# Kernel tuning notes

Hardware: AMD Instinct MI355X
Metric: run time of the kernel (lower is better)

Reference implementation:

```python
import jax, jax.numpy as jnp
import numpy as np

B, S, FEAT, HID, H = 8, 1024, 1024, 1024, 8
DH = HID // H  # head dim = 128
MASK_VAL = -128.0  # mask_val = -2**7 (soft additive mask, per original code)


def setup_inputs() -> dict:
    key = jax.random.key(0)
    ks = jax.random.split(key, 4)
    scale = 0.02
    return {
        "queries": jax.random.normal(ks[0], (B, S, FEAT), dtype=jnp.float32),
        "Wq": jax.random.normal(ks[1], (FEAT, HID), dtype=jnp.float32) * scale,
        "bq": jnp.zeros((HID,), dtype=jnp.float32),
        "Wk": jax.random.normal(ks[2], (FEAT, HID), dtype=jnp.float32) * scale,
        "bk": jnp.zeros((HID,), dtype=jnp.float32),
        "Wv": jax.random.normal(ks[3], (FEAT, HID), dtype=jnp.float32) * scale,
        "bv": jnp.zeros((HID,), dtype=jnp.float32),
    }


def reference(queries, Wq, bq, Wk, bk, Wv, bv):
    # Self-attention: keys = values = queries (torch forward defaults)
    q = queries @ Wq + bq  # [B,S,HID]
    k = queries @ Wk + bk
    v = queries @ Wv + bv
    # split heads: chunk along last dim == reshape (B,S,H,DH)
    qh = q.reshape(B, S, H, DH)
    kh = k.reshape(B, S, H, DH)
    vh = v.reshape(B, S, H, DH)
    # exp-scaled-dot score (non-standard: exp BEFORE mask/softmax)
    logits = jnp.einsum("bqhd,bkhd->bhqk", qh, kh) / np.float32(np.sqrt(DH))
    score = jnp.exp(logits)
    # soft additive causal mask: upper triangle (diag=1) gets -128
    mask = jnp.triu(jnp.full((S, S), MASK_VAL, dtype=score.dtype), k=1)
    att = jax.nn.softmax(score + mask, axis=-1)  # [B,H,S,S]
    ctx = jnp.einsum("bhqk,bkhd->bqhd", att, vh)  # [B,S,H,DH]
    # reverse heads: concat along last dim
    return ctx.reshape(B, S, HID)
```

## Files before the change

kernel.cpp:

```cpp
#include <hip/hip_runtime.h>


typedef __bf16 bf16x8 __attribute__((ext_vector_type(8)));
typedef float floatx4 __attribute__((ext_vector_type(4)));
typedef unsigned short u16;

#define RSCALE 0.08838834764831845f

__device__ __forceinline__ u16 f2b(float f) {
  union { float f; unsigned u; } v; v.f = f;
  return (u16)((v.u + 0x7FFFu + ((v.u >> 16) & 1u)) >> 16);
}

__device__ __forceinline__ void gld_lds16(const void* g, void* l) {
  __builtin_amdgcn_global_load_lds(
      (const __attribute__((address_space(1))) unsigned*)g,
      (__attribute__((address_space(3))) unsigned*)l, 16, 0, 0);
}

#define MFMA16(a, b, c) __builtin_amdgcn_mfma_f32_16x16x32_bf16(a, b, c, 0, 0, 0)

__global__ __launch_bounds__(256) void cast_x_kernel(const float4* __restrict__ X,
                                                     u16* __restrict__ Xb) {
  unsigned i = blockIdx.x * 256u + threadIdx.x;
  float4 v = X[i];
  ushort4 o;
  o.x = f2b(v.x); o.y = f2b(v.y); o.z = f2b(v.z); o.w = f2b(v.w);
  *reinterpret_cast<ushort4*>(Xb + 4u * i) = o;
}

__global__ __launch_bounds__(256) void transpose_w_kernel(
    const float* __restrict__ Wq, const float* __restrict__ Wk,
    const float* __restrict__ Wv, u16* __restrict__ Wtb) {
  const float* W = (blockIdx.z == 0) ? Wq : (blockIdx.z == 1) ? Wk : Wv;
  u16* Wt = Wtb + (size_t)blockIdx.z * (1024u * 1024u);
  __shared__ u16 tile[32][33];
  const int x = threadIdx.x, y = threadIdx.y;
  const int kt = blockIdx.x * 32, nt = blockIdx.y * 32;
#pragma unroll
  for (int i = 0; i < 4; ++i)
    tile[y + 8 * i][x] = f2b(W[(size_t)(kt + y + 8 * i) * 1024 + nt + x]);
  __syncthreads();
#pragma unroll
  for (int i = 0; i < 4; ++i)
    Wt[(size_t)(nt + y + 8 * i) * 1024 + kt + x] = tile[x][y + 8 * i];
}

__global__ __launch_bounds__(256) void gemm_qkv_kernel(
    const u16* __restrict__ Xb, const u16* __restrict__ Wtb,
    const float* __restrict__ bq, const float* __restrict__ bk,
    const float* __restrict__ bv, u16* __restrict__ Qh, u16* __restrict__ Kh,
    u16* __restrict__ Vt) {
  const int mat = blockIdx.z;
  const u16* __restrict__ Wt = Wtb + (size_t)mat * (1024u * 1024u);
  const float* __restrict__ bias = (mat == 0) ? bq : (mat == 1) ? bk : bv;

  const int m0 = blockIdx.x * 128;
  const int n0 = blockIdx.y * 128;

  __shared__ u16 As[128 * 32];
  __shared__ u16 Bs[128 * 32];

  const int tid = threadIdx.x;
  const int wid = tid >> 6;
  const int lane = tid & 63;
  const int quad = lane >> 4;
  const int l16 = lane & 15;
  const int wm = (wid & 1) * 64;
  const int wn = (wid >> 1) * 64;

  const floatx4 z4 = {0.f, 0.f, 0.f, 0.f};
  floatx4 acc[4][4];
#pragma unroll
  for (int i = 0; i < 4; ++i)
#pragma unroll
    for (int j = 0; j < 4; ++j) acc[i][j] = z4;

  const int rbase = wid * 32;
  for (int k0 = 0; k0 < 1024; k0 += 32) {
    __syncthreads();
#pragma unroll
    for (int c = 0; c < 2; ++c) {
      const int row = rbase + c * 16 + (lane >> 2);
      const int kk = k0 + (lane & 3) * 8;
      gld_lds16(Xb + (size_t)(m0 + row) * 1024 + kk, As + (rbase + c * 16) * 32);
      gld_lds16(Wt + (size_t)(n0 + row) * 1024 + kk, Bs + (rbase + c * 16) * 32);
    }
    __syncthreads();

    bf16x8 af[4], bfr[4];
#pragma unroll
    for (int i = 0; i < 4; ++i)
      af[i] = *(const bf16x8*)(As + (wm + i * 16 + l16) * 32 + quad * 8);
#pragma unroll
    for (int j = 0; j < 4; ++j)
      bfr[j] = *(const bf16x8*)(Bs + (wn + j * 16 + l16) * 32 + quad * 8);
#pragma unroll
    for (int i = 0; i < 4; ++i)
#pragma unroll
      for (int j = 0; j < 4; ++j) acc[i][j] = MFMA16(af[i], bfr[j], acc[i][j]);
  }

  const int b = m0 >> 10;
  const int h = n0 >> 7;
  const int sbase = (m0 & 1023) + wm;
  float bv4[4];
#pragma unroll
  for (int j = 0; j < 4; ++j) bv4[j] = bias[n0 + wn + j * 16 + l16];

  if (mat < 2) {
    u16* outp = (mat == 0 ? Qh : Kh) + (size_t)(b * 8 + h) * 1024 * 128;
#pragma unroll
    for (int i = 0; i < 4; ++i)
#pragma unroll
      for (int j = 0; j < 4; ++j) {
        const int d = wn + j * 16 + l16;
#pragma unroll
        for (int r = 0; r < 4; ++r) {
          const int s = sbase + i * 16 + quad * 4 + r;
          outp[(size_t)s * 128 + d] = f2b(acc[i][j][r] + bv4[j]);
        }
      }
  } else {
    u16* outp = Vt + (size_t)(b * 8 + h) * 128 * 1024;
#pragma unroll
    for (int i = 0; i < 4; ++i)
#pragma unroll
      for (int j = 0; j < 4; ++j) {
        const int d = wn + j * 16 + l16;
        const int s = sbase + i * 16 + quad * 4;
        ushort4 pk;
        pk.x = f2b(acc[i][j][0] + bv4[j]);
        pk.y = f2b(acc[i][j][1] + bv4[j]);
        pk.z = f2b(acc[i][j][2] + bv4[j]);
        pk.w = f2b(acc[i][j][3] + bv4[j]);
        *(ushort4*)(outp + (size_t)d * 1024 + s) = pk;
      }
  }
}

__global__ __launch_bounds__(256) void attn_kernel(const u16* __restrict__ Qh,
                                                   const u16* __restrict__ Kh,
                                                   const u16* __restrict__ Vt,
                                                   float* __restrict__ out) {
  const int bh = blockIdx.x;
  const int q0 = blockIdx.y * 128;
  const int tid = threadIdx.x;
  const int wid = tid >> 6;
  const int lane = tid & 63;
  const int quad = lane >> 4;
  const int l16 = lane & 15;

  __shared__ u16 Ks[32 * 128];
  __shared__ u16 Vs[128 * 32];
  __shared__ u16 Ps[4 * 32 * 32];

  const u16* __restrict__ Qbase = Qh + (size_t)bh * 1024 * 128;
  const u16* __restrict__ Kbase = Kh + (size_t)bh * 1024 * 128;
  const u16* __restrict__ Vbase = Vt + (size_t)bh * 128 * 1024;

  const int qw = q0 + wid * 32;

  bf16x8 qf[2][4];
#pragma unroll
  for (int mt = 0; mt < 2; ++mt)
#pragma unroll
    for (int c = 0; c < 4; ++c)
      qf[mt][c] = *(const bf16x8*)(Qbase + (size_t)(qw + mt * 16 + l16) * 128 +
                                   c * 32 + quad * 8);

  const floatx4 z4 = {0.f, 0.f, 0.f, 0.f};
  floatx4 o[2][8];
#pragma unroll
  for (int mt = 0; mt < 2; ++mt)
#pragma unroll
    for (int dt = 0; dt < 8; ++dt) o[mt][dt] = z4;
  float lacc[2][4] = {};

  const int kend = q0 + 128;
  for (int k0 = 0; k0 < kend; k0 += 32) {
    __syncthreads();
#pragma unroll
    for (int c = 0; c < 2; ++c) {
      const int row = wid * 8 + c * 4 + (lane >> 4);
      const int gb = (lane & 15) ^ (row & 15);
      gld_lds16(Kbase + (size_t)(k0 + row) * 128 + gb * 8,
                Ks + (wid * 8 + c * 4) * 128);
    }
#pragma unroll
    for (int c = 0; c < 2; ++c) {
      const int row = wid * 32 + c * 16 + (lane >> 2);
      const int kk = k0 + (lane & 3) * 8;
      gld_lds16(Vbase + (size_t)row * 1024 + kk, Vs + (wid * 32 + c * 16) * 32);
    }
    __syncthreads();

    bf16x8 kf[2][4];
#pragma unroll
    for (int nt = 0; nt < 2; ++nt)
#pragma unroll
      for (int c = 0; c < 4; ++c)
        kf[nt][c] = *(const bf16x8*)(Ks + (nt * 16 + l16) * 128 +
                                     (((c * 4 + quad) ^ l16) * 8));

#pragma unroll
    for (int mt = 0; mt < 2; ++mt) {
      floatx4 s0 = z4, s1 = z4;
#pragma unroll
      for (int c = 0; c < 4; ++c) {
        s0 = MFMA16(qf[mt][c], kf[0][c], s0);
        s1 = MFMA16(qf[mt][c], kf[1][c], s1);
      }
#pragma unroll
      for (int r = 0; r < 4; ++r) {
        const int qrow = qw + mt * 16 + quad * 4 + r;
        const float e0 = fminf(__expf(s0[r] * RSCALE), 85.f);
        const float e1 = fminf(__expf(s1[r] * RSCALE), 85.f);
        const float p0 = (k0 + l16 > qrow) ? 0.f : __expf(e0);
        const float p1 = (k0 + 16 + l16 > qrow) ? 0.f : __expf(e1);
        lacc[mt][r] += p0 + p1;
        Ps[wid * 1024 + (mt * 16 + quad * 4 + r) * 32 + l16] = f2b(p0);
        Ps[wid * 1024 + (mt * 16 + quad * 4 + r) * 32 + 16 + l16] = f2b(p1);
      }
    }
    asm volatile("s_waitcnt lgkmcnt(0)" ::: "memory");

    bf16x8 pa[2];
#pragma unroll
    for (int mt = 0; mt < 2; ++mt)
      pa[mt] = *(const bf16x8*)(Ps + wid * 1024 + (mt * 16 + l16) * 32 + quad * 8);
#pragma unroll
    for (int dt = 0; dt < 8; ++dt) {
      const bf16x8 vf = *(const bf16x8*)(Vs + (dt * 16 + l16) * 32 + quad * 8);
      o[0][dt] = MFMA16(pa[0], vf, o[0][dt]);
      o[1][dt] = MFMA16(pa[1], vf, o[1][dt]);
    }
  }

  float linv[2][4];
#pragma unroll
  for (int mt = 0; mt < 2; ++mt)
#pragma unroll
    for (int r = 0; r < 4; ++r) {
      float s = lacc[mt][r];
      s += __shfl_xor(s, 1, 16);
      s += __shfl_xor(s, 2, 16);
      s += __shfl_xor(s, 4, 16);
      s += __shfl_xor(s, 8, 16);
      linv[mt][r] = 1.0f / s;
    }

  float* outp = out + ((size_t)(bh >> 3) * 1024) * 1024 + (bh & 7) * 128;
#pragma unroll
  for (int mt = 0; mt < 2; ++mt)
#pragma unroll
    for (int dt = 0; dt < 8; ++dt)
#pragma unroll
      for (int r = 0; r < 4; ++r) {
        const int qrow = qw + mt * 16 + quad * 4 + r;
        outp[(size_t)qrow * 1024 + dt * 16 + l16] = o[mt][dt][r] * linv[mt][r];
      }
}

extern "C" void kernel_launch(void* const* d_in, const int* in_sizes, int n_in,
                              void* d_out, int out_size, void* d_ws,
                              size_t ws_size, hipStream_t stream) {
  const float* X = (const float*)d_in[0];
  const float* Wq = (const float*)d_in[1];
  const float* bq = (const float*)d_in[2];
  const float* Wk = (const float*)d_in[3];
  const float* bk = (const float*)d_in[4];
  const float* Wv = (const float*)d_in[5];
  const float* bv = (const float*)d_in[6];
  float* out = (float*)d_out;

  char* ws = (char*)d_ws;
  u16* Xb  = (u16*)(ws);
  u16* Wtb = (u16*)(ws + (16u << 20));
  u16* Qh  = (u16*)(ws + (22u << 20));
  u16* Kh  = (u16*)(ws + (38u << 20));
  u16* Vt  = (u16*)(ws + (54u << 20));

  cast_x_kernel<<<8192, 256, 0, stream>>>((const float4*)X, Xb);
  dim3 gt(32, 32, 3), bt(32, 8);
  transpose_w_kernel<<<gt, bt, 0, stream>>>(Wq, Wk, Wv, Wtb);
  dim3 gg(64, 8, 3);
  gemm_qkv_kernel<<<gg, 256, 0, stream>>>(Xb, Wtb, bq, bk, bv, Qh, Kh, Vt);
  dim3 ga(64, 8);
  attn_kernel<<<ga, 256, 0, stream>>>(Qh, Kh, Vt, out);
}
```

Baseline: 225.7 us.

## Merge prep kernels, widen GEMM K-tile with swizzle, single-wave attention blocks

Fuses the X cast and weight transpose into one launch. The QKV GEMM now uses a K-tile of 64 with an XOR-swizzled LDS layout, and swaps MFMA operands for Q/K so the epilogue can write packed 4-element rows. Attention is rewritten to one 64-thread wave per 32-query tile, launched longest-first across 2048 blocks. K and V fragments are read straight from global memory instead of staged through LDS, and output is stored as float4. This aims to improve causal load balance and drop block-wide barriers, at the cost of no LDS reuse of K/V across waves.

```diff
diff --git a/kernel.cpp b/kernel.cpp
--- a/kernel.cpp
+++ b/kernel.cpp
@@ -4,6 +4,7 @@
 typedef __bf16 bf16x8 __attribute__((ext_vector_type(8)));
 typedef float floatx4 __attribute__((ext_vector_type(4)));
 typedef unsigned short u16;
+typedef unsigned int u32;
 
 #define RSCALE 0.08838834764831845f
 
@@ -20,30 +21,33 @@
 
 #define MFMA16(a, b, c) __builtin_amdgcn_mfma_f32_16x16x32_bf16(a, b, c, 0, 0, 0)
 
-__global__ __launch_bounds__(256) void cast_x_kernel(const float4* __restrict__ X,
-                                                     u16* __restrict__ Xb) {
-  unsigned i = blockIdx.x * 256u + threadIdx.x;
-  float4 v = X[i];
-  ushort4 o;
-  o.x = f2b(v.x); o.y = f2b(v.y); o.z = f2b(v.z); o.w = f2b(v.w);
-  *reinterpret_cast<ushort4*>(Xb + 4u * i) = o;
-}
-
-__global__ __launch_bounds__(256) void transpose_w_kernel(
+__global__ __launch_bounds__(256) void prep_kernel(
+    const float4* __restrict__ X, u16* __restrict__ Xb,
     const float* __restrict__ Wq, const float* __restrict__ Wk,
     const float* __restrict__ Wv, u16* __restrict__ Wtb) {
-  const float* W = (blockIdx.z == 0) ? Wq : (blockIdx.z == 1) ? Wk : Wv;
-  u16* Wt = Wtb + (size_t)blockIdx.z * (1024u * 1024u);
-  __shared__ u16 tile[32][33];
-  const int x = threadIdx.x, y = threadIdx.y;
-  const int kt = blockIdx.x * 32, nt = blockIdx.y * 32;
-#pragma unroll
-  for (int i = 0; i < 4; ++i)
-    tile[y + 8 * i][x] = f2b(W[(size_t)(kt + y + 8 * i) * 1024 + nt + x]);
-  __syncthreads();
-#pragma unroll
-  for (int i = 0; i < 4; ++i)
-    Wt[(size_t)(nt + y + 8 * i) * 1024 + kt + x] = tile[x][y + 8 * i];
+  if (blockIdx.x < 8192) {
+    unsigned i = blockIdx.x * 256u + threadIdx.x;
+    float4 v = X[i];
+    ushort4 o;
+    o.x = f2b(v.x); o.y = f2b(v.y); o.z = f2b(v.z); o.w = f2b(v.w);
+    *reinterpret_cast<ushort4*>(Xb + 4u * i) = o;
+  } else {
+    const int bid = blockIdx.x - 8192;
+    const int mat = bid >> 10;
+    const int bx = bid & 31, by = (bid >> 5) & 31;
+    const float* W = (mat == 0) ? Wq : (mat == 1) ? Wk : Wv;
+    u16* Wt = Wtb + (size_t)mat * (1024u * 1024u);
+    __shared__ u16 tile[32][33];
+    const int x = threadIdx.x & 31, y = threadIdx.x >> 5;
+    const int kt = bx * 32, nt = by * 32;
+#pragma unroll
+    for (int i = 0; i < 4; ++i)
+      tile[y + 8 * i][x] = f2b(W[(size_t)(kt + y + 8 * i) * 1024 + nt + x]);
+    __syncthreads();
+#pragma unroll
+    for (int i = 0; i < 4; ++i)
+      Wt[(size_t)(nt + y + 8 * i) * 1024 + kt + x] = tile[x][y + 8 * i];
+  }
 }
 
 __global__ __launch_bounds__(256) void gemm_qkv_kernel(
@@ -52,20 +56,22 @@
     const float* __restrict__ bv, u16* __restrict__ Qh, u16* __restrict__ Kh,
     u16* __restrict__ Vt) {
   const int mat = blockIdx.z;
+  const bool matQK = (mat < 2);
   const u16* __restrict__ Wt = Wtb + (size_t)mat * (1024u * 1024u);
   const float* __restrict__ bias = (mat == 0) ? bq : (mat == 1) ? bk : bv;
 
   const int m0 = blockIdx.x * 128;
   const int n0 = blockIdx.y * 128;
 
-  __shared__ u16 As[128 * 32];
-  __shared__ u16 Bs[128 * 32];
+  __shared__ u16 As[128 * 64];
+  __shared__ u16 Bs[128 * 64];
 
   const int tid = threadIdx.x;
   const int wid = tid >> 6;
   const int lane = tid & 63;
   const int quad = lane >> 4;
   const int l16 = lane & 15;
+  const int l8 = lane & 7;
   const int wm = (wid & 1) * 64;
   const int wn = (wid >> 1) * 64;
 
@@ -76,53 +82,77 @@
 #pragma unroll
     for (int j = 0; j < 4; ++j) acc[i][j] = z4;
 
-  const int rbase = wid * 32;
-  for (int k0 = 0; k0 < 1024; k0 += 32) {
+  const int srow = wid * 32;
+  const int lrow = lane >> 3;
+  const int gblk = l8 ^ lrow;
+
+  for (int k0 = 0; k0 < 1024; k0 += 64) {
     __syncthreads();
 #pragma unroll
+    for (int c = 0; c < 4; ++c) {
+      const int row = srow + c * 8 + lrow;
+      gld_lds16(Xb + (size_t)(m0 + row) * 1024 + k0 + gblk * 8,
+                As + (srow + c * 8) * 64);
+      gld_lds16(Wt + (size_t)(n0 + row) * 1024 + k0 + gblk * 8,
+                Bs + (srow + c * 8) * 64);
+    }
+    __syncthreads();
+
+#pragma unroll
     for (int c = 0; c < 2; ++c) {
-      const int row = rbase + c * 16 + (lane >> 2);
-      const int kk = k0 + (lane & 3) * 8;
-      gld_lds16(Xb + (size_t)(m0 + row) * 1024 + kk, As + (rbase + c * 16) * 32);
-      gld_lds16(Wt + (size_t)(n0 + row) * 1024 + kk, Bs + (rbase + c * 16) * 32);
-    }
-    __syncthreads();
-
-    bf16x8 af[4], bfr[4];
-#pragma unroll
-    for (int i = 0; i < 4; ++i)
-      af[i] = *(const bf16x8*)(As + (wm + i * 16 + l16) * 32 + quad * 8);
-#pragma unroll
-    for (int j = 0; j < 4; ++j)
-      bfr[j] = *(const bf16x8*)(Bs + (wn + j * 16 + l16) * 32 + quad * 8);
-#pragma unroll
-    for (int i = 0; i < 4; ++i)
-#pragma unroll
-      for (int j = 0; j < 4; ++j) acc[i][j] = MFMA16(af[i], bfr[j], acc[i][j]);
+      const int phys = ((c * 4 + quad) ^ (l16 & 7)) * 8;
+      bf16x8 af[4], bfr[4];
+#pragma unroll
+      for (int i = 0; i < 4; ++i)
+        af[i] = *(const bf16x8*)(As + (wm + i * 16 + l16) * 64 + phys);
+#pragma unroll
+      for (int j = 0; j < 4; ++j)
+        bfr[j] = *(const bf16x8*)(Bs + (wn + j * 16 + l16) * 64 + phys);
+      if (matQK) {
+#pragma unroll
+        for (int i = 0; i < 4; ++i)
+#pragma unroll
+          for (int j = 0; j < 4; ++j)
+            acc[i][j] = MFMA16(bfr[j], af[i], acc[i][j]);
+      } else {
+#pragma unroll
+        for (int i = 0; i < 4; ++i)
+#pragma unroll
+          for (int j = 0; j < 4; ++j)
+            acc[i][j] = MFMA16(af[i], bfr[j], acc[i][j]);
+      }
+    }
   }
 
   const int b = m0 >> 10;
   const int h = n0 >> 7;
-  const int sbase = (m0 & 1023) + wm;
-  float bv4[4];
-#pragma unroll
-  for (int j = 0; j < 4; ++j) bv4[j] = bias[n0 + wn + j * 16 + l16];
-
-  if (mat < 2) {
+
+  if (matQK) {
     u16* outp = (mat == 0 ? Qh : Kh) + (size_t)(b * 8 + h) * 1024 * 128;
-#pragma unroll
-    for (int i = 0; i < 4; ++i)
+    float4 bias4[4];
+#pragma unroll
+    for (int j = 0; j < 4; ++j)
+      bias4[j] = *(const float4*)(bias + n0 + wn + j * 16 + quad * 4);
+#pragma unroll
+    for (int i = 0; i < 4; ++i) {
+      const int s = (m0 & 1023) + wm + i * 16 + l16;
 #pragma unroll
       for (int j = 0; j < 4; ++j) {
-        const int d = wn + j * 16 + l16;
-#pragma unroll
-        for (int r = 0; r < 4; ++r) {
-          const int s = sbase + i * 16 + quad * 4 + r;
-          outp[(size_t)s * 128 + d] = f2b(acc[i][j][r] + bv4[j]);
-        }
+        const int d0 = wn + j * 16 + quad * 4;
+        ushort4 pk;
+        pk.x = f2b(acc[i][j][0] + bias4[j].x);
+        pk.y = f2b(acc[i][j][1] + bias4[j].y);
+        pk.z = f2b(acc[i][j][2] + bias4[j].z);
+        pk.w = f2b(acc[i][j][3] + bias4[j].w);
+        *(ushort4*)(outp + (size_t)s * 128 + d0) = pk;
       }
+    }
   } else {
     u16* outp = Vt + (size_t)(b * 8 + h) * 128 * 1024;
+    const int sbase = (m0 & 1023) + wm;
+    float bv4[4];
+#pragma unroll
+    for (int j = 0; j < 4; ++j) bv4[j] = bias[n0 + wn + j * 16 + l16];
 #pragma unroll
     for (int i = 0; i < 4; ++i)
 #pragma unroll
@@ -139,127 +169,114 @@
   }
 }
 
-__global__ __launch_bounds__(256) void attn_kernel(const u16* __restrict__ Qh,
-                                                   const u16* __restrict__ Kh,
-                                                   const u16* __restrict__ Vt,
-                                                   float* __restrict__ out) {
-  const int bh = blockIdx.x;
-  const int q0 = blockIdx.y * 128;
-  const int tid = threadIdx.x;
-  const int wid = tid >> 6;
-  const int lane = tid & 63;
+__global__ __launch_bounds__(64, 3) void attn_kernel(const u16* __restrict__ Qh,
+                                                     const u16* __restrict__ Kh,
+                                                     const u16* __restrict__ Vt,
+                                                     float* __restrict__ out) {
+  const int id = blockIdx.x;
+  const int bh = (id & 7) * 8 + ((id >> 3) & 7);
+  const int qidx = 31 - (id >> 6);
+  const int qw = qidx * 32;
+
+  const int lane = threadIdx.x & 63;
   const int quad = lane >> 4;
   const int l16 = lane & 15;
 
-  __shared__ u16 Ks[32 * 128];
-  __shared__ u16 Vs[128 * 32];
-  __shared__ u16 Ps[4 * 32 * 32];
+  __shared__ u16 Ps[32 * 32];
 
   const u16* __restrict__ Qbase = Qh + (size_t)bh * 1024 * 128;
   const u16* __restrict__ Kbase = Kh + (size_t)bh * 1024 * 128;
   const u16* __restrict__ Vbase = Vt + (size_t)bh * 128 * 1024;
 
-  const int qw = q0 + wid * 32;
-
   bf16x8 qf[2][4];
 #pragma unroll
-  for (int mt = 0; mt < 2; ++mt)
+  for (int nt = 0; nt < 2; ++nt)
 #pragma unroll
     for (int c = 0; c < 4; ++c)
-      qf[mt][c] = *(const bf16x8*)(Qbase + (size_t)(qw + mt * 16 + l16) * 128 +
+      qf[nt][c] = *(const bf16x8*)(Qbase + (size_t)(qw + nt * 16 + l16) * 128 +
                                    c * 32 + quad * 8);
 
   const floatx4 z4 = {0.f, 0.f, 0.f, 0.f};
-  floatx4 o[2][8];
-#pragma unroll
-  for (int mt = 0; mt < 2; ++mt)
-#pragma unroll
-    for (int dt = 0; dt < 8; ++dt) o[mt][dt] = z4;
-  float lacc[2][4] = {};
-
-  const int kend = q0 + 128;
-  for (int k0 = 0; k0 < kend; k0 += 32) {
-    __syncthreads();
-#pragma unroll
-    for (int c = 0; c < 2; ++c) {
-      const int row = wid * 8 + c * 4 + (lane >> 4);
-      const int gb = (lane & 15) ^ (row & 15);
-      gld_lds16(Kbase + (size_t)(k0 + row) * 128 + gb * 8,
-                Ks + (wid * 8 + c * 4) * 128);
-    }
-#pragma unroll
-    for (int c = 0; c < 2; ++c) {
-      const int row = wid * 32 + c * 16 + (lane >> 2);
-      const int kk = k0 + (lane & 3) * 8;
-      gld_lds16(Vbase + (size_t)row * 1024 + kk, Vs + (wid * 32 + c * 16) * 32);
-    }
-    __syncthreads();
-
+  floatx4 o[8][2];
+#pragma unroll
+  for (int dt = 0; dt < 8; ++dt) { o[dt][0] = z4; o[dt][1] = z4; }
+  float lacc[2] = {0.f, 0.f};
+
+  const int psw = (quad >> 1) ^ (l16 & 3);
+  const int psr = quad ^ (l16 & 3);
+
+  for (int k0 = 0; k0 <= qw; k0 += 32) {
     bf16x8 kf[2][4];
 #pragma unroll
+    for (int f = 0; f < 2; ++f)
+#pragma unroll
+      for (int c = 0; c < 4; ++c)
+        kf[f][c] = *(const bf16x8*)(Kbase +
+                                    (size_t)(k0 + f * 16 + l16) * 128 +
+                                    c * 32 + quad * 8);
+
+#pragma unroll
+    for (int f = 0; f < 2; ++f)
+#pragma unroll
+      for (int nt = 0; nt < 2; ++nt) {
+        floatx4 st = z4;
+#pragma unroll
+        for (int c = 0; c < 4; ++c) st = MFMA16(kf[f][c], qf[nt][c], st);
+        const int qrow = qw + nt * 16 + l16;
+        const int kb = k0 + f * 16 + quad * 4;
+        float p[4];
+#pragma unroll
+        for (int r = 0; r < 4; ++r) {
+          const float e = fminf(__expf(st[r] * RSCALE), 85.f);
+          p[r] = (kb + r > qrow) ? 0.f : __expf(e);
+        }
+        lacc[nt] += (p[0] + p[1]) + (p[2] + p[3]);
+        uint2 pk;
+        pk.x = (u32)f2b(p[0]) | ((u32)f2b(p[1]) << 16);
+        pk.y = (u32)f2b(p[2]) | ((u32)f2b(p[3]) << 16);
+        *(uint2*)((char*)Ps + (nt * 16 + l16) * 64 +
+                  ((f * 2 + (quad >> 1)) ^ (l16 & 3)) * 16 + (quad & 1) * 8) = pk;
+      }
+    asm volatile("s_waitcnt lgkmcnt(0)" ::: "memory");
+
+    bf16x8 pa[2];
+#pragma unroll
     for (int nt = 0; nt < 2; ++nt)
-#pragma unroll
-      for (int c = 0; c < 4; ++c)
-        kf[nt][c] = *(const bf16x8*)(Ks + (nt * 16 + l16) * 128 +
-                                     (((c * 4 + quad) ^ l16) * 8));
-
-#pragma unroll
-    for (int mt = 0; mt < 2; ++mt) {
-      floatx4 s0 = z4, s1 = z4;
-#pragma unroll
-      for (int c = 0; c < 4; ++c) {
-        s0 = MFMA16(qf[mt][c], kf[0][c], s0);
-        s1 = MFMA16(qf[mt][c], kf[1][c], s1);
-      }
-#pragma unroll
-      for (int r = 0; r < 4; ++r) {
-        const int qrow = qw + mt * 16 + quad * 4 + r;
-        const float e0 = fminf(__expf(s0[r] * RSCALE), 85.f);
-        const float e1 = fminf(__expf(s1[r] * RSCALE), 85.f);
-        const float p0 = (k0 + l16 > qrow) ? 0.f : __expf(e0);
-        const float p1 = (k0 + 16 + l16 > qrow) ? 0.f : __expf(e1);
-        lacc[mt][r] += p0 + p1;
-        Ps[wid * 1024 + (mt * 16 + quad * 4 + r) * 32 + l16] = f2b(p0);
-        Ps[wid * 1024 + (mt * 16 + quad * 4 + r) * 32 + 16 + l16] = f2b(p1);
-      }
-    }
-    asm volatile("s_waitcnt lgkmcnt(0)" ::: "memory");
-
-    bf16x8 pa[2];
-#pragma unroll
-    for (int mt = 0; mt < 2; ++mt)
-      pa[mt] = *(const bf16x8*)(Ps + wid * 1024 + (mt * 16 + l16) * 32 + quad * 8);
+      pa[nt] = *(const bf16x8*)((char*)Ps + (nt * 16 + l16) * 64 + psr * 16);
 #pragma unroll
     for (int dt = 0; dt < 8; ++dt) {
-      const bf16x8 vf = *(const bf16x8*)(Vs + (dt * 16 + l16) * 32 + quad * 8);
-      o[0][dt] = MFMA16(pa[0], vf, o[0][dt]);
-      o[1][dt] = MFMA16(pa[1], vf, o[1][dt]);
-    }
-  }
-
-  float linv[2][4];
-#pragma unroll
-  for (int mt = 0; mt < 2; ++mt)
-#pragma unroll
-    for (int r = 0; r < 4; ++r) {
-      float s = lacc[mt][r];
-      s += __shfl_xor(s, 1, 16);
-      s += __shfl_xor(s, 2, 16);
-      s += __shfl_xor(s, 4, 16);
-      s += __shfl_xor(s, 8, 16);
-      linv[mt][r] = 1.0f / s;
-    }
-
-  float* outp = out + ((size_t)(bh >> 3) * 1024) * 1024 + (bh & 7) * 128;
-#pragma unroll
-  for (int mt = 0; mt < 2; ++mt)
-#pragma unroll
-    for (int dt = 0; dt < 8; ++dt)
-#pragma unroll
-      for (int r = 0; r < 4; ++r) {
-        const int qrow = qw + mt * 16 + quad * 4 + r;
-        outp[(size_t)qrow * 1024 + dt * 16 + l16] = o[mt][dt][r] * linv[mt][r];
-      }
+      const bf16x8 vf = *(const bf16x8*)(Vbase +
+                                         (size_t)(dt * 16 + l16) * 1024 +
+                                         k0 + quad * 8);
+      o[dt][0] = MFMA16(vf, pa[0], o[dt][0]);
+      o[dt][1] = MFMA16(vf, pa[1], o[dt][1]);
+    }
+  }
+  (void)psw;
+
+  float linv[2];
+#pragma unroll
+  for (int nt = 0; nt < 2; ++nt) {
+    float s = lacc[nt];
+    s += __shfl_xor(s, 16);
+    s += __shfl_xor(s, 32);
+    linv[nt] = 1.0f / s;
+  }
+
+  float* outp = out + (size_t)(bh >> 3) * 1024 * 1024 + (bh & 7) * 128;
+#pragma unroll
+  for (int nt = 0; nt < 2; ++nt) {
+    const int qrow = qw + nt * 16 + l16;
+#pragma unroll
+    for (int dt = 0; dt < 8; ++dt) {
+      float4 v;
+      v.x = o[dt][nt][0] * linv[nt];
+      v.y = o[dt][nt][1] * linv[nt];
+      v.z = o[dt][nt][2] * linv[nt];
+      v.w = o[dt][nt][3] * linv[nt];
+      *(float4*)(outp + (size_t)qrow * 1024 + dt * 16 + quad * 4) = v;
+    }
+  }
 }
 
 extern "C" void kernel_launch(void* const* d_in, const int* in_sizes, int n_in,
@@ -281,11 +298,9 @@
   u16* Kh  = (u16*)(ws + (38u << 20));
   u16* Vt  = (u16*)(ws + (54u << 20));
 
-  cast_x_kernel<<<8192, 256, 0, stream>>>((const float4*)X, Xb);
-  dim3 gt(32, 32, 3), bt(32, 8);
-  transpose_w_kernel<<<gt, bt, 0, stream>>>(Wq, Wk, Wv, Wtb);
+  prep_kernel<<<8192 + 3072, 256, 0, stream>>>((const float4*)X, Xb, Wq, Wk,
+                                               Wv, Wtb);
   dim3 gg(64, 8, 3);
   gemm_qkv_kernel<<<gg, 256, 0, stream>>>(Xb, Wtb, bq, bk, bv, Qh, Kh, Vt);
-  dim3 ga(64, 8);
-  attn_kernel<<<ga, 256, 0, stream>>>(Qh, Kh, Vt, out);
-}
+  attn_kernel<<<2048, 64, 0, stream>>>(Qh, Kh, Vt, out);
+}
```

New measurement: 292.3 us. +29.5%, slower.
